# Optimization experiments

Measured on AMD Instinct MI355X. Metric: run time of the kernel, lower is better.

Reference implementation:

```python
import jax, jax.numpy as jnp
import numpy as np

H, D = 8, 16          # heads, per-head dim (hidden 128 = H*D)
IN_C, HID, OUT_C = 128, 128, 64
NG, ND = 100000, 50000
EG, EDG = 800000, 800000
NEG_SLOPE = 0.2


def setup_inputs() -> dict:
    key = jax.random.key(0)
    ks = jax.random.split(key, 20)
    inp = {}
    inp['x_gene'] = jax.random.normal(ks[0], (NG, IN_C), jnp.float32)
    inp['x_disease'] = jax.random.normal(ks[1], (ND, IN_C), jnp.float32)
    inp['eg_src'] = jax.random.randint(ks[2], (EG,), 0, NG, jnp.int32)
    inp['eg_dst'] = jax.random.randint(ks[3], (EG,), 0, NG, jnp.int32)
    inp['edg_src'] = jax.random.randint(ks[4], (EDG,), 0, ND, jnp.int32)
    inp['edg_dst'] = jax.random.randint(ks[5], (EDG,), 0, NG, jnp.int32)
    s = 1.0 / np.sqrt(IN_C)
    inp['W_gene'] = jax.random.normal(ks[6], (IN_C, HID), jnp.float32) * s
    inp['b_gene'] = jnp.zeros((HID,), jnp.float32)
    inp['W_dis'] = jax.random.normal(ks[7], (IN_C, HID), jnp.float32) * s
    inp['b_dis'] = jnp.zeros((HID,), jnp.float32)
    inp['att_src_gg'] = jax.random.normal(ks[8], (H, D), jnp.float32) * 0.1
    inp['att_dst_gg'] = jax.random.normal(ks[9], (H, D), jnp.float32) * 0.1
    inp['att_src_dg'] = jax.random.normal(ks[10], (H, D), jnp.float32) * 0.1
    inp['att_dst_dg'] = jax.random.normal(ks[11], (H, D), jnp.float32) * 0.1
    inp['Wk'] = jax.random.normal(ks[12], (HID, HID), jnp.float32) * (1.0 / np.sqrt(HID))
    inp['bk'] = jnp.zeros((HID,), jnp.float32)
    inp['q'] = jax.random.normal(ks[13], (HID,), jnp.float32) * 0.1
    inp['W_lin'] = jax.random.normal(ks[14], (HID, OUT_C), jnp.float32) * (1.0 / np.sqrt(HID))
    inp['b_lin'] = jnp.zeros((OUT_C,), jnp.float32)
    return inp


def _edge_attn(xs, xd, src, dst, a_s, a_d, n_dst):
    # xs:[Ns,H,D] projected src feats, xd:[Nd,H,D]; GAT-style per-edge-type attention
    e_src = (xs * a_s).sum(-1)                      # [Ns,H]
    e_dst = (xd * a_d).sum(-1)                      # [Nd,H]
    alpha = jax.nn.leaky_relu(e_src[src] + e_dst[dst], NEG_SLOPE)   # [E,H]
    m = jax.ops.segment_max(alpha, dst, num_segments=n_dst)
    m = jnp.where(jnp.isfinite(m), m, 0.0)
    ex = jnp.exp(alpha - m[dst])
    denom = jax.ops.segment_sum(ex, dst, num_segments=n_dst)
    w = ex / (denom[dst] + 1e-16)                   # softmax over incoming edges
    msg = xs[src] * w[..., None]                    # [E,H,D]
    out = jax.ops.segment_sum(msg, dst, num_segments=n_dst)  # [Nd,H,D]
    return jax.nn.relu(out.reshape(n_dst, H * D))


def reference(x_gene, x_disease, eg_src, eg_dst, edg_src, edg_dst,
              W_gene, b_gene, W_dis, b_dis,
              att_src_gg, att_dst_gg, att_src_dg, att_dst_dg,
              Wk, bk, q, W_lin, b_lin):
    ng = x_gene.shape[0]
    hg = (x_gene @ W_gene + b_gene).reshape(ng, H, D)
    hd = (x_disease @ W_dis + b_dis).reshape(-1, H, D)
    # metapath aggregations landing on 'gene'
    out_gg = _edge_attn(hg, hg, eg_src, eg_dst, att_src_gg, att_dst_gg, ng)
    out_dg = _edge_attn(hd, hg, edg_src, edg_dst, att_src_dg, att_dst_dg, ng)
    outs = jnp.stack([out_gg, out_dg])              # [K=2, Ng, HID]
    # semantic-level attention
    score = (jnp.tanh(outs @ Wk + bk).mean(1) * q).sum(-1)   # [K]
    beta = jax.nn.softmax(score)
    gene = (beta[:, None, None] * outs).sum(0)      # [Ng, HID]
    return gene @ W_lin + b_lin                     # [Ng, OUT_C]
```

## Files before the change

kernel.cpp:

```cpp
#include <hip/hip_runtime.h>
#include <cstdint>
#include <cstddef>

#define NEG_SLOPE 0.2f
#define BSHIFT 8

typedef __attribute__((ext_vector_type(8))) short short8;
typedef __attribute__((ext_vector_type(4))) float f32x4;

__device__ __forceinline__ float leakyf(float x) { return x > 0.f ? x : NEG_SLOPE * x; }
__device__ __forceinline__ float fast_tanh(float x) {
    float e = __expf(2.f * x);
    return 1.f - 2.f / (e + 1.f);
}
__device__ __forceinline__ unsigned short f2bf(float x) {
    unsigned u = __float_as_uint(x);
    unsigned r = u + 0x7FFFu + ((u >> 16) & 1u);
    return (unsigned short)(r >> 16);
}

__global__ void bext_kernel(const float* __restrict__ W, const float* __restrict__ bias,
                            const float* __restrict__ att0, const float* __restrict__ att1,
                            const float* __restrict__ att2,
                            unsigned short* __restrict__ BExt, float* __restrict__ beArr)
{
    const int t = threadIdx.x;
    for (int task = t; task < 128 * 128; task += 256) {
        int col = task >> 7, k = task & 127;
        BExt[(size_t)col * 128 + k] = f2bf(W[(size_t)k * 128 + col]);
    }
    for (int task = t; task < 32 * 128; task += 256) {
        int col = task >> 7, k = task & 127;
        int vec = col >> 3, h = col & 7;
        const float* att = (vec == 0) ? att0 : (vec == 1) ? att1 : (vec == 2) ? att2 : nullptr;
        float s = 0.f;
        if (att) {
            #pragma unroll
            for (int d = 0; d < 16; ++d) s = fmaf(W[(size_t)k * 128 + h * 16 + d], att[h * 16 + d], s);
        }
        BExt[(size_t)(128 + col) * 128 + k] = f2bf(s);
    }
    if (t < 24) {
        int vec = t >> 3, h = t & 7;
        const float* att = (vec == 0) ? att0 : (vec == 1) ? att1 : att2;
        float s = 0.f;
        if (att) {
            #pragma unroll
            for (int d = 0; d < 16; ++d) s = fmaf(bias[h * 16 + d], att[h * 16 + d], s);
        }
        beArr[t] = s;
    }
}

__global__ __launch_bounds__(256) void proj_mfma(
    const float* __restrict__ x, const unsigned short* __restrict__ BExt,
    const float* __restrict__ bias, const float* __restrict__ beArr,
    unsigned short* __restrict__ hout,
    float* __restrict__ e0, float* __restrict__ e1, float* __restrict__ e2, int N)
{
    __shared__ short atile[128 * 128];
    const int t = threadIdx.x;
    const int row0 = blockIdx.x * 128;
    {
        const int row = t >> 1, q8 = t & 1;
        const int gr = row0 + row;
        #pragma unroll
        for (int c = 0; c < 8; ++c) {
            const int kc = q8 * 8 + c;
            float4 l0 = make_float4(0.f, 0.f, 0.f, 0.f), l1 = l0;
            if (gr < N) {
                l0 = *(const float4*)(x + (size_t)gr * 128 + kc * 8);
                l1 = *(const float4*)(x + (size_t)gr * 128 + kc * 8 + 4);
            }
            int4 u;
            u.x = (int)f2bf(l0.x) | ((int)f2bf(l0.y) << 16);
            u.y = (int)f2bf(l0.z) | ((int)f2bf(l0.w) << 16);
            u.z = (int)f2bf(l1.x) | ((int)f2bf(l1.y) << 16);
            u.w = (int)f2bf(l1.z) | ((int)f2bf(l1.w) << 16);
            const int chunk = row * 16 + kc;
            const int chunk_sw = chunk ^ (row & 7);
            *(int4*)((char*)atile + chunk_sw * 16) = u;
        }
    }
    __syncthreads();
    const int w = t >> 6, l = t & 63;
    const int lrow = l & 15, lk = l >> 4;
    f32x4 acc[2][10];
    #pragma unroll
    for (int a = 0; a < 2; ++a)
        #pragma unroll
        for (int ct = 0; ct < 10; ++ct) { acc[a][ct][0] = 0.f; acc[a][ct][1] = 0.f; acc[a][ct][2] = 0.f; acc[a][ct][3] = 0.f; }
    #pragma unroll
    for (int ks = 0; ks < 4; ++ks) {
        short8 afr[2];
        #pragma unroll
        for (int a = 0; a < 2; ++a) {
            const int rowl = w * 32 + a * 16 + lrow;
            const int chunk = rowl * 16 + ks * 4 + lk;
            const int chunk_sw = chunk ^ (rowl & 7);
            afr[a] = *(short8*)((char*)atile + chunk_sw * 16);
        }
        #pragma unroll
        for (int ct = 0; ct < 10; ++ct) {
            const unsigned short* bp = BExt + ((size_t)(ct * 16 + lrow) * 128 + ks * 32 + lk * 8);
            short8 bfr = *(const short8*)bp;
            acc[0][ct] = __builtin_amdgcn_mfma_f32_16x16x32_bf16(afr[0], bfr, acc[0][ct], 0, 0, 0);
            acc[1][ct] = __builtin_amdgcn_mfma_f32_16x16x32_bf16(afr[1], bfr, acc[1][ct], 0, 0, 0);
        }
    }
    #pragma unroll
    for (int ct = 0; ct < 8; ++ct) {
        const int col = ct * 16 + lrow;
        const float bv = bias[col];
        #pragma unroll
        for (int a = 0; a < 2; ++a) {
            #pragma unroll
            for (int r = 0; r < 4; ++r) {
                const int grow = row0 + w * 32 + a * 16 + lk * 4 + r;
                if (grow < N) hout[(size_t)grow * 128 + col] = f2bf(acc[a][ct][r] + bv);
            }
        }
    }
    {
        const float be = beArr[lrow];
        float* tgt = (lrow < 8) ? e0 : e1;
        const int head = lrow & 7;
        if (tgt) {
            #pragma unroll
            for (int a = 0; a < 2; ++a) {
                #pragma unroll
                for (int r = 0; r < 4; ++r) {
                    const int grow = row0 + w * 32 + a * 16 + lk * 4 + r;
                    if (grow < N) tgt[(size_t)grow * 8 + head] = acc[a][8][r] + be;
                }
            }
        }
    }
    if (lrow < 8 && e2) {
        const float be = beArr[16 + lrow];
        #pragma unroll
        for (int a = 0; a < 2; ++a) {
            #pragma unroll
            for (int r = 0; r < 4; ++r) {
                const int grow = row0 + w * 32 + a * 16 + lk * 4 + r;
                if (grow < N) e2[(size_t)grow * 8 + lrow] = acc[a][9][r] + be;
            }
        }
    }
}

__global__ __launch_bounds__(256) void bucket_hist(
    const int* __restrict__ dstg, int Eg, const int* __restrict__ dstd, int Ed,
    int NBg, int NBtot, int* __restrict__ bucketCnt)
{
    __shared__ int h[1024];
    const int t = threadIdx.x;
    for (int j = t; j < NBtot; j += 256) h[j] = 0;
    __syncthreads();
    const int Etot = Eg + Ed;
    const int base = blockIdx.x * 4096;
    #pragma unroll
    for (int k = 0; k < 16; ++k) {
        int i = base + k * 256 + t;
        if (i < Etot) {
            int b = (i < Eg) ? (dstg[i] >> BSHIFT) : NBg + (dstd[i - Eg] >> BSHIFT);
            atomicAdd(&h[b], 1);
        }
    }
    __syncthreads();
    for (int j = t; j < NBtot; j += 256) {
        int c = h[j];
        if (c) atomicAdd(&bucketCnt[j], c);
    }
}

__global__ void bucket_scan(const int* __restrict__ bucketCnt, int NBtot, int Etot,
                            int* __restrict__ bucketBase, int* __restrict__ bucketCursor)
{
    __shared__ int s[1024];
    int t = threadIdx.x;
    int v = (t < NBtot) ? bucketCnt[t] : 0;
    s[t] = v;
    __syncthreads();
    for (int o = 1; o < 1024; o <<= 1) {
        int add = (t >= o) ? s[t - o] : 0;
        __syncthreads();
        s[t] += add;
        __syncthreads();
    }
    if (t < NBtot) {
        int e = s[t] - v;
        bucketBase[t] = e;
        bucketCursor[t] = e;
    }
    if (t == 0) bucketBase[NBtot] = Etot;
}

__global__ __launch_bounds__(256) void bucket_scatter(
    const int* __restrict__ dstg, const int* __restrict__ srcg, int Eg,
    const int* __restrict__ dstd, const int* __restrict__ srcd, int Ed,
    int NBg, int NBtot, int* __restrict__ bucketCursor, unsigned* __restrict__ coarse)
{
    __shared__ int h[800];
    __shared__ int basearr[800];
    __shared__ int cur[800];
    const int t = threadIdx.x;
    for (int j = t; j < NBtot; j += 256) h[j] = 0;
    __syncthreads();
    const int Etot = Eg + Ed;
    const int base = blockIdx.x * 4096;
    int bk[16];
    unsigned pk[16];
    #pragma unroll
    for (int k = 0; k < 16; ++k) {
        int i = base + k * 256 + t;
        bk[k] = -1;
        if (i < Etot) {
            int dst, src, goff;
            if (i < Eg) { dst = dstg[i]; src = srcg[i]; goff = 0; }
            else        { dst = dstd[i - Eg]; src = srcd[i - Eg]; goff = NBg; }
            bk[k] = goff + (dst >> BSHIFT);
            pk[k] = (unsigned)src | ((unsigned)(dst & 255) << 24);
            atomicAdd(&h[bk[k]], 1);
        }
    }
    __syncthreads();
    for (int j = t; j < NBtot; j += 256) {
        int c = h[j];
        basearr[j] = c ? atomicAdd(&bucketCursor[j], c) : 0;
        cur[j] = 0;
    }
    __syncthreads();
    #pragma unroll
    for (int k = 0; k < 16; ++k) {
        if (bk[k] >= 0) {
            int r = atomicAdd(&cur[bk[k]], 1);
            coarse[basearr[bk[k]] + r] = pk[k];
        }
    }
}

__global__ __launch_bounds__(256) void bucket_sort(
    const unsigned* __restrict__ coarse, const int* __restrict__ bucketBase,
    int NBg, int Eg, int Ed, int N,
    int* __restrict__ offg, int* __restrict__ offd,
    int* __restrict__ srcs_g, int* __restrict__ srcs_d)
{
    __shared__ int hist[256];
    __shared__ int excl[256];
    __shared__ int cur[256];
    const int b = blockIdx.x;
    const int t = threadIdx.x;
    const int s0 = bucketBase[b], s1 = bucketBase[b + 1];
    const int cnt = s1 - s0;
    const bool isg = b < NBg;
    const int d0 = (isg ? b : b - NBg) << BSHIFT;
    hist[t] = 0;
    __syncthreads();
    for (int i = t; i < cnt; i += 256) {
        unsigned p = coarse[s0 + i];
        atomicAdd(&hist[p >> 24], 1);
    }
    __syncthreads();
    int v = hist[t];
    excl[t] = v;
    __syncthreads();
    for (int o = 1; o < 256; o <<= 1) {
        int add = (t >= o) ? excl[t - o] : 0;
        __syncthreads();
        excl[t] += add;
        __syncthreads();
    }
    const int e = excl[t] - v;
    const int localBase = isg ? s0 : s0 - Eg;
    const int d = d0 + t;
    if (d < N) {
        if (isg) offg[d] = localBase + e;
        else     offd[d] = localBase + e;
    }
    cur[t] = e;
    __syncthreads();
    int* outp = isg ? srcs_g : srcs_d;
    for (int i = t; i < cnt; i += 256) {
        unsigned p = coarse[s0 + i];
        int r = atomicAdd(&cur[p >> 24], 1);
        outp[localBase + r] = (int)(p & 0xFFFFFFu);
    }
    if (b == 0 && t == 0) { offg[N] = Eg; offd[N] = Ed; }
}

__global__ __launch_bounds__(256) void aggregate_kernel(
    const unsigned short* __restrict__ xs,
    const float* __restrict__ esrc,
    const float* __restrict__ edst,
    const int* __restrict__ off,
    const int* __restrict__ srcsorted,
    float* __restrict__ outp,
    int Nd)
{
    __shared__ float exbuf[4][64 * 8];
    const int lane = threadIdx.x & 63;
    const int wslot = threadIdx.x >> 6;
    const int n = blockIdx.x * 4 + wslot;
    if (n >= Nd) return;
    const int o0 = off[n], o1 = off[n + 1];
    const int deg = o1 - o0;
    const int li = lane & 31, half = lane >> 5;
    const int j0 = li * 4;
    const int hh = li >> 2;
    if (deg == 0) {
        if (half == 0) *(float4*)(outp + (size_t)n * 128 + j0) = make_float4(0.f, 0.f, 0.f, 0.f);
        return;
    }
    float ed[8];
    {
        float4 a = *(const float4*)(edst + (size_t)n * 8);
        float4 b = *(const float4*)(edst + (size_t)n * 8 + 4);
        ed[0] = a.x; ed[1] = a.y; ed[2] = a.z; ed[3] = a.w;
        ed[4] = b.x; ed[5] = b.y; ed[6] = b.z; ed[7] = b.w;
    }
    if (deg <= 64) {
        const bool act = lane < deg;
        int s = act ? srcsorted[o0 + lane] : 0;
        float exv[8];
        {
            float4 ea = make_float4(0.f, 0.f, 0.f, 0.f), eb = ea;
            if (act) {
                ea = *(const float4*)(esrc + (size_t)s * 8);
                eb = *(const float4*)(esrc + (size_t)s * 8 + 4);
            }
            float a[8] = {ea.x, ea.y, ea.z, ea.w, eb.x, eb.y, eb.z, eb.w};
            #pragma unroll
            for (int h2 = 0; h2 < 8; ++h2)
                exv[h2] = act ? __expf(leakyf(a[h2] + ed[h2])) : 0.f;
        }
        *(float4*)(&exbuf[wslot][lane * 8])     = make_float4(exv[0], exv[1], exv[2], exv[3]);
        *(float4*)(&exbuf[wslot][lane * 8 + 4]) = make_float4(exv[4], exv[5], exv[6], exv[7]);
        float4 num = make_float4(0.f, 0.f, 0.f, 0.f);
        float den = 0.f;
        const int iters = (deg + 1) >> 1;
        #pragma unroll 2
        for (int k = 0; k < iters; ++k) {
            int i = 2 * k + half;
            if (i < deg) {
                int si = __shfl(s, i);
                float wgt = exbuf[wslot][i * 8 + hh];
                int2 xv2 = *(const int2*)(xs + (size_t)si * 128 + j0);
                unsigned ux = (unsigned)xv2.x, uy = (unsigned)xv2.y;
                float x0 = __uint_as_float(ux << 16);
                float x1 = __uint_as_float(ux & 0xFFFF0000u);
                float x2 = __uint_as_float(uy << 16);
                float x3 = __uint_as_float(uy & 0xFFFF0000u);
                num.x = fmaf(wgt, x0, num.x);
                num.y = fmaf(wgt, x1, num.y);
                num.z = fmaf(wgt, x2, num.z);
                num.w = fmaf(wgt, x3, num.w);
                den += wgt;
            }
        }
        num.x += __shfl_xor(num.x, 32);
        num.y += __shfl_xor(num.y, 32);
        num.z += __shfl_xor(num.z, 32);
        num.w += __shfl_xor(num.w, 32);
        den += __shfl_xor(den, 32);
        if (half == 0) {
            float inv = 1.f / (den + 1e-16f);
            float4 r;
            r.x = fmaxf(num.x * inv, 0.f);
            r.y = fmaxf(num.y * inv, 0.f);
            r.z = fmaxf(num.z * inv, 0.f);
            r.w = fmaxf(num.w * inv, 0.f);
            *(float4*)(outp + (size_t)n * 128 + j0) = r;
        }
        return;
    }
    {
        const int j0b = lane * 2;
        const int h = lane >> 3;
        float edh;
        {
            float u4a = (h & 4) ? ed[4] : ed[0];
            float u4b = (h & 4) ? ed[5] : ed[1];
            float u4c = (h & 4) ? ed[6] : ed[2];
            float u4d = (h & 4) ? ed[7] : ed[3];
            float u2a = (h & 2) ? u4c : u4a;
            float u2b = (h & 2) ? u4d : u4b;
            edh = (h & 1) ? u2b : u2a;
        }
        float den = 0.f, num0 = 0.f, num1 = 0.f;
        for (int base = 0; base < deg; base += 64) {
            int ii = base + lane;
            bool act = ii < deg;
            int sreg = srcsorted[o0 + (act ? ii : 0)];
            int cl = deg - base;
            if (cl > 64) cl = 64;
            for (int i = 0; i < cl; ++i) {
                int s = __shfl(sreg, i);
                float ev = esrc[(size_t)s * 8 + h];
                float ex = __expf(leakyf(ev + edh));
                unsigned uv = *(const unsigned*)(xs + (size_t)s * 128 + j0b);
                float x0 = __uint_as_float(uv << 16);
                float x1 = __uint_as_float(uv & 0xFFFF0000u);
                num0 = fmaf(ex, x0, num0);
                num1 = fmaf(ex, x1, num1);
                den += ex;
            }
        }
        float inv = 1.f / (den + 1e-16f);
        float r0 = num0 * inv, r1 = num1 * inv;
        r0 = r0 > 0.f ? r0 : 0.f;
        r1 = r1 > 0.f ? r1 : 0.f;
        *(float2*)(outp + (size_t)n * 128 + j0b) = make_float2(r0, r1);
    }
}

__global__ void wkt_kernel(const float* __restrict__ Wk, unsigned short* __restrict__ WkT) {
    int c = threadIdx.x;
    for (int k = 0; k < 128; ++k)
        WkT[c * 128 + k] = f2bf(Wk[(size_t)k * 128 + c]);
}

__global__ __launch_bounds__(256) void score2_mfma(
    const float* __restrict__ gg, const float* __restrict__ dg,
    const unsigned short* __restrict__ WkT,
    const float* __restrict__ bk, const float* __restrict__ q,
    float* __restrict__ scoreAcc, int N)
{
    __shared__ short atile[128 * 128];
    __shared__ float sred[4];
    const int t = threadIdx.x;
    const int row0 = blockIdx.x * 64;
    {
        const int row = t >> 1, q8 = t & 1;
        const int gr = row0 + (row & 63);
        const float* srcp = (row < 64) ? gg : dg;
        #pragma unroll
        for (int c = 0; c < 8; ++c) {
            const int kc = q8 * 8 + c;
            float4 l0 = make_float4(0.f, 0.f, 0.f, 0.f), l1 = l0;
            if (gr < N) {
                l0 = *(const float4*)(srcp + (size_t)gr * 128 + kc * 8);
                l1 = *(const float4*)(srcp + (size_t)gr * 128 + kc * 8 + 4);
            }
            int4 u;
            u.x = (int)f2bf(l0.x) | ((int)f2bf(l0.y) << 16);
            u.y = (int)f2bf(l0.z) | ((int)f2bf(l0.w) << 16);
            u.z = (int)f2bf(l1.x) | ((int)f2bf(l1.y) << 16);
            u.w = (int)f2bf(l1.z) | ((int)f2bf(l1.w) << 16);
            const int chunk = row * 16 + kc;
            const int chunk_sw = chunk ^ (row & 7);
            *(int4*)((char*)atile + chunk_sw * 16) = u;
        }
    }
    __syncthreads();
    const int w = t >> 6, l = t & 63;
    const int lrow = l & 15, lk = l >> 4;
    f32x4 acc[2][8];
    #pragma unroll
    for (int a = 0; a < 2; ++a)
        #pragma unroll
        for (int ct = 0; ct < 8; ++ct) { acc[a][ct][0] = 0.f; acc[a][ct][1] = 0.f; acc[a][ct][2] = 0.f; acc[a][ct][3] = 0.f; }
    #pragma unroll
    for (int ks = 0; ks < 4; ++ks) {
        short8 afr[2];
        #pragma unroll
        for (int a = 0; a < 2; ++a) {
            const int rowl = w * 32 + a * 16 + lrow;
            const int chunk = rowl * 16 + ks * 4 + lk;
            const int chunk_sw = chunk ^ (rowl & 7);
            afr[a] = *(short8*)((char*)atile + chunk_sw * 16);
        }
        #pragma unroll
        for (int ct = 0; ct < 8; ++ct) {
            const unsigned short* bp = WkT + ((size_t)(ct * 16 + lrow) * 128 + ks * 32 + lk * 8);
            short8 bfr = *(const short8*)bp;
            acc[0][ct] = __builtin_amdgcn_mfma_f32_16x16x32_bf16(afr[0], bfr, acc[0][ct], 0, 0, 0);
            acc[1][ct] = __builtin_amdgcn_mfma_f32_16x16x32_bf16(afr[1], bfr, acc[1][ct], 0, 0, 0);
        }
    }
    float s = 0.f;
    #pragma unroll
    for (int ct = 0; ct < 8; ++ct) {
        const int col = ct * 16 + lrow;
        const float bkv = bk[col];
        const float qv = q[col];
        #pragma unroll
        for (int a = 0; a < 2; ++a) {
            #pragma unroll
            for (int r = 0; r < 4; ++r) {
                const int rloc = a * 16 + lk * 4 + r;
                const int grow = row0 + ((w * 32 + rloc) & 63);
                if (grow < N) s = fmaf(fast_tanh(acc[a][ct][r] + bkv), qv, s);
            }
        }
    }
    #pragma unroll
    for (int o = 1; o < 64; o <<= 1) s += __shfl_xor(s, o);
    if (l == 0) sred[w] = s;
    __syncthreads();
    if (t == 0) {
        float pg = sred[0] + sred[1];
        float pd = sred[2] + sred[3];
        int slot = blockIdx.x & 63;
        atomicAdd(&scoreAcc[slot], pg);
        atomicAdd(&scoreAcc[64 + slot], pd);
    }
}

__global__ void beta_kernel(float* __restrict__ scoreAcc, float invN) {
    int t = threadIdx.x;
    float v0 = scoreAcc[t];
    float v1 = scoreAcc[64 + t];
    #pragma unroll
    for (int o = 1; o < 64; o <<= 1) {
        v0 += __shfl_xor(v0, o);
        v1 += __shfl_xor(v1, o);
    }
    if (t == 0) {
        float s0 = v0 * invN, s1 = v1 * invN;
        float mx = fmaxf(s0, s1);
        float e0 = __expf(s0 - mx), e1 = __expf(s1 - mx);
        float inv = 1.f / (e0 + e1);
        scoreAcc[128] = e0 * inv;
        scoreAcc[129] = e1 * inv;
    }
}

__global__ __launch_bounds__(256) void final_kernel(
    const float* __restrict__ gg, const float* __restrict__ dg,
    const float* __restrict__ beta,
    const float* __restrict__ Wl, const float* __restrict__ bl,
    float* __restrict__ outp, int N)
{
    __shared__ float wlds[128 * 64];
    __shared__ float glds[32 * 128];
    const int t = threadIdx.x;
    #pragma unroll
    for (int p = 0; p < 8; ++p) {
        int idx = (t + 256 * p) * 4;
        *(float4*)(wlds + idx) = *(const float4*)(Wl + idx);
    }
    const float bet0 = beta[0], bet1 = beta[1];
    const int row0 = blockIdx.x * 32;
    #pragma unroll
    for (int p = 0; p < 4; ++p) {
        int idx = t + 256 * p;
        int r = idx >> 5;
        int c4 = idx & 31;
        float4 a = make_float4(0.f, 0.f, 0.f, 0.f), b = a, g;
        if (row0 + r < N) {
            a = *(const float4*)(gg + (size_t)(row0 + r) * 128 + c4 * 4);
            b = *(const float4*)(dg + (size_t)(row0 + r) * 128 + c4 * 4);
        }
        g.x = bet0 * a.x + bet1 * b.x;
        g.y = bet0 * a.y + bet1 * b.y;
        g.z = bet0 * a.z + bet1 * b.z;
        g.w = bet0 * a.w + bet1 * b.w;
        *(float4*)(glds + r * 128 + c4 * 4) = g;
    }
    __syncthreads();
    const int rg = t >> 5, ct = t & 31;
    float acc[4][2];
    {
        float2 bv = *(const float2*)(bl + ct * 2);
        #pragma unroll
        for (int rr = 0; rr < 4; ++rr) { acc[rr][0] = bv.x; acc[rr][1] = bv.y; }
    }
    #pragma unroll 2
    for (int i = 0; i < 128; i += 4) {
        float4 xv[4];
        #pragma unroll
        for (int rr = 0; rr < 4; ++rr) xv[rr] = *(const float4*)(glds + (rg + 8 * rr) * 128 + i);
        #pragma unroll
        for (int qq = 0; qq < 4; ++qq) {
            float2 wv = *(const float2*)(wlds + (i + qq) * 64 + ct * 2);
            #pragma unroll
            for (int rr = 0; rr < 4; ++rr) {
                float xs = ((const float*)&xv[rr])[qq];
                acc[rr][0] = fmaf(xs, wv.x, acc[rr][0]);
                acc[rr][1] = fmaf(xs, wv.y, acc[rr][1]);
            }
        }
    }
    #pragma unroll
    for (int rr = 0; rr < 4; ++rr) {
        int grow = row0 + rg + 8 * rr;
        if (grow < N)
            *(float2*)(outp + (size_t)grow * 64 + ct * 2) = make_float2(acc[rr][0], acc[rr][1]);
    }
}

extern "C" void kernel_launch(void* const* d_in, const int* in_sizes, int n_in,
                              void* d_out, int out_size, void* d_ws, size_t ws_size,
                              hipStream_t stream) {
    (void)n_in; (void)out_size; (void)ws_size;
    const float* x_gene = (const float*)d_in[0];
    const float* x_dis  = (const float*)d_in[1];
    const int* eg_src   = (const int*)d_in[2];
    const int* eg_dst   = (const int*)d_in[3];
    const int* edg_src  = (const int*)d_in[4];
    const int* edg_dst  = (const int*)d_in[5];
    const float* W_gene = (const float*)d_in[6];
    const float* b_gene = (const float*)d_in[7];
    const float* W_dis  = (const float*)d_in[8];
    const float* b_dis  = (const float*)d_in[9];
    const float* att_src_gg = (const float*)d_in[10];
    const float* att_dst_gg = (const float*)d_in[11];
    const float* att_src_dg = (const float*)d_in[12];
    const float* att_dst_dg = (const float*)d_in[13];
    const float* Wk    = (const float*)d_in[14];
    const float* bk    = (const float*)d_in[15];
    const float* q     = (const float*)d_in[16];
    const float* W_lin = (const float*)d_in[17];
    const float* b_lin = (const float*)d_in[18];
    float* out = (float*)d_out;

    const int NG_ = in_sizes[0] / 128;
    const int ND_ = in_sizes[1] / 128;
    const int EG_ = in_sizes[2];
    const int EDG_ = in_sizes[4];

    char* w = (char*)d_ws;
    auto alloc = [&](size_t bytes) -> char* {
        char* p = w;
        w += (bytes + 255) & ~(size_t)255;
        return p;
    };
    unsigned short* hg = (unsigned short*)alloc((size_t)NG_ * 128 * 2);
    unsigned short* hd = (unsigned short*)alloc((size_t)ND_ * 128 * 2);
    float* e_src_gg = (float*)alloc((size_t)NG_ * 8 * 4);
    float* e_dst_gg = (float*)alloc((size_t)NG_ * 8 * 4);
    float* e_dst_dg = (float*)alloc((size_t)NG_ * 8 * 4);
    float* e_src_dg = (float*)alloc((size_t)ND_ * 8 * 4);
    float* out_gg   = (float*)alloc((size_t)NG_ * 128 * 4);
    float* out_dg   = (float*)alloc((size_t)NG_ * 128 * 4);
    int* offg  = (int*)alloc((size_t)(NG_ + 1) * 4);
    int* offd  = (int*)alloc((size_t)(NG_ + 1) * 4);
    int* srcs_g = (int*)alloc((size_t)EG_ * 4);
    int* srcs_d = (int*)alloc((size_t)EDG_ * 4);
    unsigned* coarse = (unsigned*)alloc((size_t)(EG_ + EDG_) * 4);
    int* bucketCnt    = (int*)alloc(4096);
    int* bucketBase   = (int*)alloc(4096);
    int* bucketCursor = (int*)alloc(4096);
    unsigned short* WkT   = (unsigned short*)alloc(128 * 128 * 2);
    unsigned short* bextg = (unsigned short*)alloc(160 * 128 * 2);
    unsigned short* bextd = (unsigned short*)alloc(160 * 128 * 2);
    float* beg = (float*)alloc(128);
    float* bed = (float*)alloc(128);
    float* score = (float*)alloc(1024);

    const int NBg = (NG_ + 255) >> BSHIFT;
    const int NBtot = 2 * NBg;
    const int Etot = EG_ + EDG_;
    const int nbE = (Etot + 4095) / 4096;

    bext_kernel<<<1, 256, 0, stream>>>(W_gene, b_gene,
        att_src_gg, att_dst_gg, att_dst_dg, bextg, beg);
    bext_kernel<<<1, 256, 0, stream>>>(W_dis, b_dis,
        att_src_dg, (const float*)nullptr, (const float*)nullptr, bextd, bed);
    wkt_kernel<<<1, 128, 0, stream>>>(Wk, WkT);

    proj_mfma<<<(NG_ + 127) / 128, 256, 0, stream>>>(
        x_gene, bextg, b_gene, beg, hg, e_src_gg, e_dst_gg, e_dst_dg, NG_);
    proj_mfma<<<(ND_ + 127) / 128, 256, 0, stream>>>(
        x_dis, bextd, b_dis, bed, hd, e_src_dg, (float*)nullptr, (float*)nullptr, ND_);

    hipMemsetAsync(bucketCnt, 0, (size_t)NBtot * 4, stream);
    bucket_hist<<<nbE, 256, 0, stream>>>(eg_dst, EG_, edg_dst, EDG_, NBg, NBtot, bucketCnt);
    bucket_scan<<<1, 1024, 0, stream>>>(bucketCnt, NBtot, Etot, bucketBase, bucketCursor);
    bucket_scatter<<<nbE, 256, 0, stream>>>(
        eg_dst, eg_src, EG_, edg_dst, edg_src, EDG_, NBg, NBtot, bucketCursor, coarse);
    bucket_sort<<<NBtot, 256, 0, stream>>>(
        coarse, bucketBase, NBg, EG_, EDG_, NG_, offg, offd, srcs_g, srcs_d);

    aggregate_kernel<<<(NG_ + 3) / 4, 256, 0, stream>>>(
        hg, e_src_gg, e_dst_gg, offg, srcs_g, out_gg, NG_);
    aggregate_kernel<<<(NG_ + 3) / 4, 256, 0, stream>>>(
        hd, e_src_dg, e_dst_dg, offd, srcs_d, out_dg, NG_);

    hipMemsetAsync(score, 0, 512, stream);
    score2_mfma<<<(NG_ + 63) / 64, 256, 0, stream>>>(out_gg, out_dg, WkT, bk, q, score, NG_);
    beta_kernel<<<1, 64, 0, stream>>>(score, 1.0f / (float)NG_);

    final_kernel<<<(NG_ + 31) / 32, 256, 0, stream>>>(
        out_gg, out_dg, score + 128, W_lin, b_lin, out, NG_);
}
```

Before: 413.4 us.

## Merge paired projection and aggregation launches, parallelize weight prep, transpose MFMA output

The weight-extension kernel now runs across 20 blocks instead of one. The gene and disease projections are merged into a single launch, and so are the two edge-type aggregations, with each block picking its input set from its block index. The MFMA operands in the projection are swapped so each lane holds one row with four consecutive columns, which allows packed 8-byte bf16 stores instead of scattered 2-byte stores. This is meant to cut launch overhead and tail underutilization and to improve store coalescing. The cost is extra per-block branching on pointer selection.

After: 363.8 us. -12.0%, faster.

```diff
diff --git a/kernel.cpp b/kernel.cpp
--- a/kernel.cpp
+++ b/kernel.cpp
@@ -19,28 +19,31 @@
     return (unsigned short)(r >> 16);
 }
 
-__global__ void bext_kernel(const float* __restrict__ W, const float* __restrict__ bias,
-                            const float* __restrict__ att0, const float* __restrict__ att1,
-                            const float* __restrict__ att2,
-                            unsigned short* __restrict__ BExt, float* __restrict__ beArr)
+__global__ void bext2_kernel(const float* __restrict__ W, const float* __restrict__ bias,
+                             const float* __restrict__ att0, const float* __restrict__ att1,
+                             const float* __restrict__ att2,
+                             unsigned short* __restrict__ BExt, float* __restrict__ beArr)
 {
     const int t = threadIdx.x;
-    for (int task = t; task < 128 * 128; task += 256) {
-        int col = task >> 7, k = task & 127;
-        BExt[(size_t)col * 128 + k] = f2bf(W[(size_t)k * 128 + col]);
-    }
-    for (int task = t; task < 32 * 128; task += 256) {
-        int col = task >> 7, k = task & 127;
-        int vec = col >> 3, h = col & 7;
-        const float* att = (vec == 0) ? att0 : (vec == 1) ? att1 : (vec == 2) ? att2 : nullptr;
-        float s = 0.f;
-        if (att) {
-            #pragma unroll
-            for (int d = 0; d < 16; ++d) s = fmaf(W[(size_t)k * 128 + h * 16 + d], att[h * 16 + d], s);
-        }
-        BExt[(size_t)(128 + col) * 128 + k] = f2bf(s);
-    }
-    if (t < 24) {
+    const int cg = blockIdx.x;
+    for (int task = t; task < 1024; task += 256) {
+        int col = cg * 8 + (task >> 7);
+        int k = task & 127;
+        float v;
+        if (col < 128) {
+            v = W[(size_t)k * 128 + col];
+        } else {
+            int ec = col - 128, vec = ec >> 3, h = ec & 7;
+            const float* att = (vec == 0) ? att0 : (vec == 1) ? att1 : (vec == 2) ? att2 : nullptr;
+            v = 0.f;
+            if (att) {
+                #pragma unroll
+                for (int d = 0; d < 16; ++d) v = fmaf(W[(size_t)k * 128 + h * 16 + d], att[h * 16 + d], v);
+            }
+        }
+        BExt[(size_t)col * 128 + k] = f2bf(v);
+    }
+    if (cg == 0 && t < 24) {
         int vec = t >> 3, h = t & 7;
         const float* att = (vec == 0) ? att0 : (vec == 1) ? att1 : att2;
         float s = 0.f;
@@ -52,15 +55,29 @@
     }
 }
 
-__global__ __launch_bounds__(256) void proj_mfma(
-    const float* __restrict__ x, const unsigned short* __restrict__ BExt,
-    const float* __restrict__ bias, const float* __restrict__ beArr,
-    unsigned short* __restrict__ hout,
-    float* __restrict__ e0, float* __restrict__ e1, float* __restrict__ e2, int N)
+__global__ __launch_bounds__(256) void proj_mfma2(
+    const float* __restrict__ xg, const unsigned short* __restrict__ bextg,
+    const float* __restrict__ biasg, const float* __restrict__ beg,
+    unsigned short* __restrict__ hgp, float* __restrict__ e0g, float* __restrict__ e1g,
+    float* __restrict__ e2g, int NG, int nbG,
+    const float* __restrict__ xd, const unsigned short* __restrict__ bextd,
+    const float* __restrict__ biasd, const float* __restrict__ bed,
+    unsigned short* __restrict__ hdp, float* __restrict__ e0d, int ND)
 {
     __shared__ short atile[128 * 128];
     const int t = threadIdx.x;
-    const int row0 = blockIdx.x * 128;
+    const bool isG = blockIdx.x < nbG;
+    const int blk = isG ? blockIdx.x : blockIdx.x - nbG;
+    const float* x = isG ? xg : xd;
+    const unsigned short* BExt = isG ? bextg : bextd;
+    const float* bias = isG ? biasg : biasd;
+    const float* beArr = isG ? beg : bed;
+    unsigned short* hout = isG ? hgp : hdp;
+    float* e0 = isG ? e0g : e0d;
+    float* e1 = isG ? e1g : (float*)nullptr;
+    float* e2 = isG ? e2g : (float*)nullptr;
+    const int N = isG ? NG : ND;
+    const int row0 = blk * 128;
     {
         const int row = t >> 1, q8 = t & 1;
         const int gr = row0 + row;
@@ -92,58 +109,49 @@
         for (int ct = 0; ct < 10; ++ct) { acc[a][ct][0] = 0.f; acc[a][ct][1] = 0.f; acc[a][ct][2] = 0.f; acc[a][ct][3] = 0.f; }
     #pragma unroll
     for (int ks = 0; ks < 4; ++ks) {
-        short8 afr[2];
+        short8 xfr[2];
         #pragma unroll
         for (int a = 0; a < 2; ++a) {
             const int rowl = w * 32 + a * 16 + lrow;
             const int chunk = rowl * 16 + ks * 4 + lk;
             const int chunk_sw = chunk ^ (rowl & 7);
-            afr[a] = *(short8*)((char*)atile + chunk_sw * 16);
+            xfr[a] = *(short8*)((char*)atile + chunk_sw * 16);
         }
         #pragma unroll
         for (int ct = 0; ct < 10; ++ct) {
             const unsigned short* bp = BExt + ((size_t)(ct * 16 + lrow) * 128 + ks * 32 + lk * 8);
-            short8 bfr = *(const short8*)bp;
-            acc[0][ct] = __builtin_amdgcn_mfma_f32_16x16x32_bf16(afr[0], bfr, acc[0][ct], 0, 0, 0);
-            acc[1][ct] = __builtin_amdgcn_mfma_f32_16x16x32_bf16(afr[1], bfr, acc[1][ct], 0, 0, 0);
-        }
-    }
-    #pragma unroll
-    for (int ct = 0; ct < 8; ++ct) {
-        const int col = ct * 16 + lrow;
-        const float bv = bias[col];
-        #pragma unroll
-        for (int a = 0; a < 2; ++a) {
+            short8 wfr = *(const short8*)bp;
+            acc[0][ct] = __builtin_amdgcn_mfma_f32_16x16x32_bf16(wfr, xfr[0], acc[0][ct], 0, 0, 0);
+            acc[1][ct] = __builtin_amdgcn_mfma_f32_16x16x32_bf16(wfr, xfr[1], acc[1][ct], 0, 0, 0);
+        }
+    }
+    #pragma unroll
+    for (int a = 0; a < 2; ++a) {
+        const int grow = row0 + w * 32 + a * 16 + lrow;
+        if (grow < N) {
+            #pragma unroll
+            for (int ct = 0; ct < 8; ++ct) {
+                const int col = ct * 16 + lk * 4;
+                float4 bv = *(const float4*)(bias + col);
+                int2 u;
+                u.x = (int)f2bf(acc[a][ct][0] + bv.x) | ((int)f2bf(acc[a][ct][1] + bv.y) << 16);
+                u.y = (int)f2bf(acc[a][ct][2] + bv.z) | ((int)f2bf(acc[a][ct][3] + bv.w) << 16);
+                *(int2*)(hout + (size_t)grow * 128 + col) = u;
+            }
             #pragma unroll
             for (int r = 0; r < 4; ++r) {
-                const int grow = row0 + w * 32 + a * 16 + lk * 4 + r;
-                if (grow < N) hout[(size_t)grow * 128 + col] = f2bf(acc[a][ct][r] + bv);
-            }
-        }
-    }
-    {
-        const float be = beArr[lrow];
-        float* tgt = (lrow < 8) ? e0 : e1;
-        const int head = lrow & 7;
-        if (tgt) {
-            #pragma unroll
-            for (int a = 0; a < 2; ++a) {
+                const int ecol = lk * 4 + r;
+                const int head = ecol & 7;
+                float v = acc[a][8][r] + beArr[ecol];
+                if (ecol < 8) { if (e0) e0[(size_t)grow * 8 + head] = v; }
+                else          { if (e1) e1[(size_t)grow * 8 + head] = v; }
+            }
+            if (e2) {
                 #pragma unroll
                 for (int r = 0; r < 4; ++r) {
-                    const int grow = row0 + w * 32 + a * 16 + lk * 4 + r;
-                    if (grow < N) tgt[(size_t)grow * 8 + head] = acc[a][8][r] + be;
+                    const int ecol = lk * 4 + r;
+                    if (ecol < 8) e2[(size_t)grow * 8 + ecol] = acc[a][9][r] + beArr[16 + ecol];
                 }
-            }
-        }
-    }
-    if (lrow < 8 && e2) {
-        const float be = beArr[16 + lrow];
-        #pragma unroll
-        for (int a = 0; a < 2; ++a) {
-            #pragma unroll
-            for (int r = 0; r < 4; ++r) {
-                const int grow = row0 + w * 32 + a * 16 + lk * 4 + r;
-                if (grow < N) e2[(size_t)grow * 8 + lrow] = acc[a][9][r] + be;
             }
         }
     }
@@ -289,19 +297,27 @@
     if (b == 0 && t == 0) { offg[N] = Eg; offd[N] = Ed; }
 }
 
-__global__ __launch_bounds__(256) void aggregate_kernel(
-    const unsigned short* __restrict__ xs,
-    const float* __restrict__ esrc,
-    const float* __restrict__ edst,
-    const int* __restrict__ off,
-    const int* __restrict__ srcsorted,
-    float* __restrict__ outp,
-    int Nd)
+__global__ __launch_bounds__(256) void aggregate2_kernel(
+    const unsigned short* __restrict__ xsA, const float* __restrict__ esrcA,
+    const float* __restrict__ edstA, const int* __restrict__ offA,
+    const int* __restrict__ srcA, float* __restrict__ outA,
+    const unsigned short* __restrict__ xsB, const float* __restrict__ esrcB,
+    const float* __restrict__ edstB, const int* __restrict__ offB,
+    const int* __restrict__ srcB, float* __restrict__ outB,
+    int Nd, int nbA)
 {
     __shared__ float exbuf[4][64 * 8];
     const int lane = threadIdx.x & 63;
     const int wslot = threadIdx.x >> 6;
-    const int n = blockIdx.x * 4 + wslot;
+    const bool isA = blockIdx.x < nbA;
+    const int blk = isA ? blockIdx.x : blockIdx.x - nbA;
+    const unsigned short* xs = isA ? xsA : xsB;
+    const float* esrc = isA ? esrcA : esrcB;
+    const float* edst = isA ? edstA : edstB;
+    const int* off = isA ? offA : offB;
+    const int* srcsorted = isA ? srcA : srcB;
+    float* outp = isA ? outA : outB;
+    const int n = blk * 4 + wslot;
     if (n >= Nd) return;
     const int o0 = off[n], o1 = off[n + 1];
     const int deg = o1 - o0;
@@ -645,8 +661,8 @@
     unsigned short* WkT   = (unsigned short*)alloc(128 * 128 * 2);
     unsigned short* bextg = (unsigned short*)alloc(160 * 128 * 2);
     unsigned short* bextd = (unsigned short*)alloc(160 * 128 * 2);
-    float* beg = (float*)alloc(128);
-    float* bed = (float*)alloc(128);
+    float* beg = (float*)alloc(256);
+    float* bed = (float*)alloc(256);
     float* score = (float*)alloc(1024);
 
     const int NBg = (NG_ + 255) >> BSHIFT;
@@ -654,16 +670,19 @@
     const int Etot = EG_ + EDG_;
     const int nbE = (Etot + 4095) / 4096;
 
-    bext_kernel<<<1, 256, 0, stream>>>(W_gene, b_gene,
+    bext2_kernel<<<20, 256, 0, stream>>>(W_gene, b_gene,
         att_src_gg, att_dst_gg, att_dst_dg, bextg, beg);
-    bext_kernel<<<1, 256, 0, stream>>>(W_dis, b_dis,
+    bext2_kernel<<<20, 256, 0, stream>>>(W_dis, b_dis,
         att_src_dg, (const float*)nullptr, (const float*)nullptr, bextd, bed);
     wkt_kernel<<<1, 128, 0, stream>>>(Wk, WkT);
 
-    proj_mfma<<<(NG_ + 127) / 128, 256, 0, stream>>>(
-        x_gene, bextg, b_gene, beg, hg, e_src_gg, e_dst_gg, e_dst_dg, NG_);
-    proj_mfma<<<(ND_ + 127) / 128, 256, 0, stream>>>(
-        x_dis, bextd, b_dis, bed, hd, e_src_dg, (float*)nullptr, (float*)nullptr, ND_);
+    {
+        const int nbG = (NG_ + 127) / 128;
+        const int nbD = (ND_ + 127) / 128;
+        proj_mfma2<<<nbG + nbD, 256, 0, stream>>>(
+            x_gene, bextg, b_gene, beg, hg, e_src_gg, e_dst_gg, e_dst_dg, NG_, nbG,
+            x_dis, bextd, b_dis, bed, hd, e_src_dg, ND_);
+    }
 
     hipMemsetAsync(bucketCnt, 0, (size_t)NBtot * 4, stream);
     bucket_hist<<<nbE, 256, 0, stream>>>(eg_dst, EG_, edg_dst, EDG_, NBg, NBtot, bucketCnt);
@@ -673,10 +692,13 @@
     bucket_sort<<<NBtot, 256, 0, stream>>>(
         coarse, bucketBase, NBg, EG_, EDG_, NG_, offg, offd, srcs_g, srcs_d);
 
-    aggregate_kernel<<<(NG_ + 3) / 4, 256, 0, stream>>>(
-        hg, e_src_gg, e_dst_gg, offg, srcs_g, out_gg, NG_);
-    aggregate_kernel<<<(NG_ + 3) / 4, 256, 0, stream>>>(
-        hd, e_src_dg, e_dst_dg, offd, srcs_d, out_dg, NG_);
+    {
+        const int nbA = (NG_ + 3) / 4;
+        aggregate2_kernel<<<2 * nbA, 256, 0, stream>>>(
+            hg, e_src_gg, e_dst_gg, offg, srcs_g, out_gg,
+            hd, e_src_dg, e_dst_dg, offd, srcs_d, out_dg,
+            NG_, nbA);
+    }
 
     hipMemsetAsync(score, 0, 512, stream);
     score2_mfma<<<(NG_ + 63) / 64, 256, 0, stream>>>(out_gg, out_dg, WkT, bk, q, score, NG_);
```
